# Optimization experiments

Hardware: AMD Instinct MI355X
Metric: run time of the kernel (lower is better)

## Reference

```python
import jax, jax.numpy as jnp
import numpy as np

N, E, F, H, RBF = 50000, 400000, 128, 8, 100
HD = F // H
CUTOFF = 6.0

def _xavier(k, shape):
    fan_out, fan_in = shape
    lim = (6.0 / (fan_in + fan_out)) ** 0.5
    return jax.random.uniform(k, shape, minval=-lim, maxval=lim, dtype=jnp.float32)

def setup_inputs():
    key = jax.random.key(0)
    ks = jax.random.split(key, 16)
    x = jax.random.normal(ks[0], (N, F), jnp.float32)
    vec = jax.random.normal(ks[1], (N, 3, F), jnp.float32)
    edge_index = jax.random.randint(ks[2], (2, E), 0, N, dtype=jnp.int32)
    r_ij = jax.random.uniform(ks[3], (E,), jnp.float32) * CUTOFF
    d_ij = jax.random.normal(ks[4], (E, 3), jnp.float32)
    d_ij = d_ij / jnp.linalg.norm(d_ij, axis=-1, keepdims=True)
    f_ij = jax.random.normal(ks[5], (E, RBF), jnp.float32)
    return dict(
        x=x, vec=vec, edge_index=edge_index, r_ij=r_ij, f_ij=f_ij, d_ij=d_ij,
        ln_w=jnp.ones((F,), jnp.float32), ln_b=jnp.zeros((F,), jnp.float32),
        Wq=_xavier(ks[6], (F, F)), bq=jnp.zeros((F,), jnp.float32),
        Wk=_xavier(ks[7], (F, F)), bk=jnp.zeros((F,), jnp.float32),
        Wv=_xavier(ks[8], (3 * F, F)), bv=jnp.zeros((3 * F,), jnp.float32),
        Wvec=_xavier(ks[9], (3 * F, F)), bvec=jnp.zeros((3 * F,), jnp.float32),
        Wo=_xavier(ks[10], (3 * F, F)), bo=jnp.zeros((3 * F,), jnp.float32),
        Wdk=_xavier(ks[11], (F, RBF)), bdk=jnp.zeros((F,), jnp.float32),
        Wdv=_xavier(ks[12], (3 * F, RBF)), bdv=jnp.zeros((3 * F,), jnp.float32),
    )

def _cutoff(r):
    # CosineCutoff with cutoff_lower=0
    return 0.5 * (jnp.cos(r * (jnp.pi / CUTOFF)) + 1.0) * (r < CUTOFF).astype(r.dtype)

def reference(x, vec, edge_index, r_ij, f_ij, d_ij, ln_w, ln_b, Wq, bq, Wk, bk,
              Wv, bv, Wvec, bvec, Wo, bo, Wdk, bdk, Wdv, bdv):
    src, dst = edge_index[0], edge_index[1]  # PyG: x_j = x[src], x_i = x[dst], aggregate at dst
    mu = x.mean(-1, keepdims=True)
    var = ((x - mu) ** 2).mean(-1, keepdims=True)
    xn = (x - mu) / jnp.sqrt(var + 1e-5) * ln_w + ln_b
    q = (xn @ Wq.T + bq).reshape(N, H, HD)
    k = (xn @ Wk.T + bk).reshape(N, H, HD)
    v = (xn @ Wv.T + bv).reshape(N, H, 3 * HD)
    vp = vec @ Wvec.T + bvec  # (N,3,3F)
    vec1, vec2, vec3 = vp[..., :F], vp[..., F:2 * F], vp[..., 2 * F:]
    vec_dot = (vec1 * vec2).sum(axis=1)  # (N,F)
    vec_h = vec.reshape(N, 3, H, HD)
    dk = jax.nn.silu(f_ij @ Wdk.T + bdk).reshape(E, H, HD)
    dv = jax.nn.silu(f_ij @ Wdv.T + bdv).reshape(E, H, 3 * HD)
    # edge-wise messages
    attn = jax.nn.silu((q[dst] * k[src] * dk).sum(-1)) * _cutoff(r_ij)[:, None]  # (E,H)
    v_j = v[src] * dv
    xm, v1m, v2m = v_j[..., :HD], v_j[..., HD:2 * HD], v_j[..., 2 * HD:]
    xm = xm * attn[..., None]  # (E,H,HD)
    vecm = vec_h[src] * v1m[:, None] + v2m[:, None] * d_ij[:, :, None, None]  # (E,3,H,HD)
    # scatter-add to destination nodes
    x_agg = jax.ops.segment_sum(xm.reshape(E, F), dst, num_segments=N)
    vec_agg = jax.ops.segment_sum(vecm.reshape(E, 3 * F), dst, num_segments=N).reshape(N, 3, F)
    o = x_agg @ Wo.T + bo
    o1, o2, o3 = o[:, :F], o[:, F:2 * F], o[:, 2 * F:]
    dx = vec_dot * o2 + o3
    dvec = vec3 * o1[:, None, :] + vec_agg
    return dx, dvec
```

## Files before the change

kernel.cpp:

```cpp
#include <hip/hip_runtime.h>

#define N_NODES 50000
#define N_EDGES 400000

typedef __bf16 bf16x8 __attribute__((ext_vector_type(8)));
typedef float f32x4 __attribute__((ext_vector_type(4)));

__device__ __forceinline__ float bflo(uint u){ union{uint i; float f;} v; v.i = u<<16; return v.f; }
__device__ __forceinline__ float bfhi(uint u){ union{uint i; float f;} v; v.i = u & 0xffff0000u; return v.f; }
__device__ __forceinline__ float bf2f(ushort u){ union{uint i; float f;} v; v.i = ((uint)u)<<16; return v.f; }
__device__ __forceinline__ ushort f2bf(float f){
  union{float f; uint i;} v; v.f = f;
  uint r = (v.i + 0x7fffu + ((v.i>>16)&1u))>>16;
  return (ushort)r;
}
__device__ __forceinline__ uint pack2(float a, float b){
  return (uint)f2bf(a) | ((uint)f2bf(b)<<16);
}

__global__ __launch_bounds__(256) void f32_to_bf16(
    const float* __restrict__ in, ushort* __restrict__ out, int n)
{
  int i = blockIdx.x*256 + threadIdx.x;
  if (i < n) out[i] = f2bf(in[i]);
}

__global__ __launch_bounds__(256) void ln_kernel(
    const float* __restrict__ x, const float* __restrict__ w,
    const float* __restrict__ b, ushort* __restrict__ xn)
{
  int n = blockIdx.x*4 + (threadIdx.x>>6);
  if (n >= N_NODES) return;
  int lane = threadIdx.x & 63;
  float2 xp = ((const float2*)x)[(size_t)n*64 + lane];
  float x0 = xp.x, x1 = xp.y;
  float s = x0 + x1, s2 = x0*x0 + x1*x1;
  #pragma unroll
  for (int off=1; off<64; off<<=1){ s += __shfl_xor(s,off); s2 += __shfl_xor(s2,off); }
  float mu  = s*(1.0f/128.0f);
  float var = s2*(1.0f/128.0f) - mu*mu;
  float inv = 1.0f/sqrtf(var + 1e-5f);
  float2 wp = ((const float2*)w)[lane];
  float2 bp = ((const float2*)b)[lane];
  float y0 = (x0-mu)*inv*wp.x + bp.x;
  float y1 = (x1-mu)*inv*wp.y + bp.y;
  ((uint*)xn)[(size_t)n*64 + lane] = pack2(y0, y1);
}

__global__ __launch_bounds__(256) void hist_kernel(
    const int* __restrict__ ei, int* __restrict__ cnt)
{
  int e = blockIdx.x*256 + threadIdx.x;
  if (e < N_EDGES) atomicAdd(&cnt[ei[N_EDGES + e]], 1);
}

__global__ __launch_bounds__(1024) void scan_kernel(
    const int* __restrict__ cnt, int* __restrict__ offs, int* __restrict__ cursor)
{
  __shared__ int wsum[16];
  __shared__ int carry_s;
  int tid = threadIdx.x, lane = tid & 63, wid = tid >> 6;
  if (tid == 0) carry_s = 0;
  __syncthreads();
  for (int base = 0; base < N_NODES; base += 1024){
    int i = base + tid;
    int v = (i < N_NODES) ? cnt[i] : 0;
    int x = v;
    #pragma unroll
    for (int o=1;o<64;o<<=1){ int t=__shfl_up(x,o); if (lane>=o) x+=t; }
    if (lane == 63) wsum[wid] = x;
    __syncthreads();
    if (wid == 0){
      int ws = (lane < 16) ? wsum[lane] : 0;
      #pragma unroll
      for (int o=1;o<16;o<<=1){ int t=__shfl_up(ws,o); if (lane>=o) ws+=t; }
      if (lane < 16) wsum[lane] = ws;
    }
    __syncthreads();
    int wpre = (wid > 0) ? wsum[wid-1] : 0;
    int exc = x + wpre - v;
    int total = wsum[15];
    int o_ = carry_s + exc;
    if (i < N_NODES){ offs[i] = o_; cursor[i] = o_; }
    __syncthreads();
    if (tid == 0) carry_s += total;
    __syncthreads();
  }
  if (tid == 0) offs[N_NODES] = carry_s;
}

__global__ __launch_bounds__(256) void scatter_kernel(
    const int* __restrict__ ei, int* __restrict__ cursor,
    int* __restrict__ perm, int* __restrict__ srcs)
{
  int e = blockIdx.x*256 + threadIdx.x;
  if (e >= N_EDGES) return;
  int d = ei[N_EDGES + e];
  int pos = atomicAdd(&cursor[d], 1);
  perm[pos] = e;
  srcs[pos] = ei[e];
}

#define LDP 40

template<int MODE, int AF32>
__global__ __launch_bounds__(256) void gemm_bt(
    const void* __restrict__ Av, const ushort* __restrict__ W,
    const ushort* __restrict__ W2,
    const float* __restrict__ bias, const float* __restrict__ bias2,
    void* Cptr, const void* aux1, void* aux2,
    int M, int K, int Nc, const int* __restrict__ ridx)
{
  __shared__ ushort As[128*LDP];
  __shared__ ushort Bs[128*LDP];
  __shared__ ushort Bs2[(MODE==7) ? 128*LDP : 2];
  const int tid = threadIdx.x;
  const int row0 = blockIdx.x*128, col0 = blockIdx.y*128;
  const int wave = tid>>6, lane = tid&63;
  const int wm = (wave>>1)*64, wn = (wave&1)*64;
  const int lr = lane&15, lq = lane>>4;
  f32x4 acc[4][4] = {};
  f32x4 acc2[4][4] = {};

  for (int k0=0; k0<K; k0+=32){
    #pragma unroll
    for (int rnd=0; rnd<2; rnd++){
      int e4 = (rnd*256 + tid)*8;
      int r = e4>>5, c = e4&31;
      int gk = k0 + c;
      {
        int gr = row0 + r;
        uint2 lo, hi;
        if (AF32){
          const float* Af = (const float*)Av;
          int ga = gr;
          if (ridx && gr < M) ga = ridx[gr];
          if (gr < M && gk + 8 <= K){
            const float* p = Af + (size_t)ga*K + gk;
            float4 f0 = *(const float4*)p;
            float4 f1 = *(const float4*)(p+4);
            lo = make_uint2(pack2(f0.x,f0.y), pack2(f0.z,f0.w));
            hi = make_uint2(pack2(f1.x,f1.y), pack2(f1.z,f1.w));
          } else {
            float t[8];
            #pragma unroll
            for (int i=0;i<8;i++) t[i] = (gr<M && gk+i<K) ? Af[(size_t)ga*K + gk + i] : 0.0f;
            lo = make_uint2(pack2(t[0],t[1]), pack2(t[2],t[3]));
            hi = make_uint2(pack2(t[4],t[5]), pack2(t[6],t[7]));
          }
        } else {
          const ushort* Ab = (const ushort*)Av;
          if (gr < M && gk + 8 <= K){
            const ushort* p = Ab + (size_t)gr*K + gk;
            lo = *(const uint2*)p; hi = *(const uint2*)(p+4);
          } else {
            ushort t[8];
            #pragma unroll
            for (int i=0;i<8;i++) t[i] = (gr<M && gk+i<K) ? Ab[(size_t)gr*K + gk + i] : (ushort)0;
            lo = make_uint2(((uint)t[0])|((uint)t[1]<<16), ((uint)t[2])|((uint)t[3]<<16));
            hi = make_uint2(((uint)t[4])|((uint)t[5]<<16), ((uint)t[6])|((uint)t[7]<<16));
          }
        }
        *(uint2*)&As[r*LDP + c]     = lo;
        *(uint2*)&As[r*LDP + c + 4] = hi;
      }
      {
        int gr = col0 + r;
        uint2 lo, hi;
        if (gr < Nc && gk + 8 <= K){
          const ushort* p = W + (size_t)gr*K + gk;
          lo = *(const uint2*)p; hi = *(const uint2*)(p+4);
        } else {
          ushort t[8];
          #pragma unroll
          for (int i=0;i<8;i++) t[i] = (gr<Nc && gk+i<K) ? W[(size_t)gr*K + gk + i] : (ushort)0;
          lo = make_uint2(((uint)t[0])|((uint)t[1]<<16), ((uint)t[2])|((uint)t[3]<<16));
          hi = make_uint2(((uint)t[4])|((uint)t[5]<<16), ((uint)t[6])|((uint)t[7]<<16));
        }
        *(uint2*)&Bs[r*LDP + c]     = lo;
        *(uint2*)&Bs[r*LDP + c + 4] = hi;
      }
      if (MODE==7){
        int gr = col0 + r;
        uint2 lo, hi;
        if (gr < Nc && gk + 8 <= K){
          const ushort* p = W2 + (size_t)gr*K + gk;
          lo = *(const uint2*)p; hi = *(const uint2*)(p+4);
        } else {
          ushort t[8];
          #pragma unroll
          for (int i=0;i<8;i++) t[i] = (gr<Nc && gk+i<K) ? W2[(size_t)gr*K + gk + i] : (ushort)0;
          lo = make_uint2(((uint)t[0])|((uint)t[1]<<16), ((uint)t[2])|((uint)t[3]<<16));
          hi = make_uint2(((uint)t[4])|((uint)t[5]<<16), ((uint)t[6])|((uint)t[7]<<16));
        }
        *(uint2*)&Bs2[r*LDP + c]     = lo;
        *(uint2*)&Bs2[r*LDP + c + 4] = hi;
      }
    }
    __syncthreads();
    bf16x8 af[4], bfr[4];
    #pragma unroll
    for (int i=0;i<4;i++) af[i]  = *(const bf16x8*)&As[(wm + i*16 + lr)*LDP + lq*8];
    #pragma unroll
    for (int i=0;i<4;i++) bfr[i] = *(const bf16x8*)&Bs[(wn + i*16 + lr)*LDP + lq*8];
    #pragma unroll
    for (int i=0;i<4;i++)
      #pragma unroll
      for (int j=0;j<4;j++)
        acc[i][j] = __builtin_amdgcn_mfma_f32_16x16x32_bf16(af[i], bfr[j], acc[i][j], 0,0,0);
    if (MODE==7){
      bf16x8 bfr2[4];
      #pragma unroll
      for (int i=0;i<4;i++) bfr2[i] = *(const bf16x8*)&Bs2[(wn + i*16 + lr)*LDP + lq*8];
      #pragma unroll
      for (int i=0;i<4;i++)
        #pragma unroll
        for (int j=0;j<4;j++)
          acc2[i][j] = __builtin_amdgcn_mfma_f32_16x16x32_bf16(af[i], bfr2[j], acc2[i][j], 0,0,0);
    }
    __syncthreads();
  }

  const ushort* aux1b = (const ushort*)aux1;
  const float*  aux1f = (const float*)aux1;
  float* aux2f = (float*)aux2;

  #pragma unroll
  for (int i=0;i<4;i++){
    int rowb = row0 + wm + i*16 + lq*4;
    #pragma unroll
    for (int j=0;j<4;j++){
      int c = col0 + wn + j*16 + lr;
      float bv  = bias  ? bias[c]  : 0.0f;
      float bv2 = (MODE==7) ? bias2[c] : 0.0f;
      #pragma unroll
      for (int rg=0; rg<4; rg++){
        int row = rowb + rg;
        if (row < M){
          float vv = acc[i][j][rg] + bv;
          size_t idx = (size_t)row*Nc + c;
          if (MODE==0){
            ((ushort*)Cptr)[idx] = f2bf(vv);
          } else if (MODE==1){
            vv = vv/(1.0f + __expf(-vv));
            ((ushort*)Cptr)[idx] = f2bf(vv);
          } else if (MODE==4){
            aux2f[idx] *= vv;
          } else if (MODE==5){
            float r = aux1f[idx] + vv;
            ((float*)Cptr)[idx] = r;
          } else if (MODE==6){
            float o1 = bf2f(aux1b[(size_t)(row/3)*Nc + c]);
            float r = vv*o1 + aux2f[idx];
            ((float*)Cptr)[idx] = r;
          } else if (MODE==7){
            float vv2 = acc2[i][j][rg] + bv2;
            atomicAdd(aux2f + (size_t)(row/3)*Nc + c, vv*vv2);
          }
        }
      }
    }
  }
}

__global__ __launch_bounds__(256) void agg_kernel(
    int st, int len,
    const int* __restrict__ offs, const int* __restrict__ srcs,
    const int* __restrict__ perm,
    const float* __restrict__ rij, const float* __restrict__ dij,
    const ushort* __restrict__ qk, const ushort* __restrict__ v,
    const ushort* __restrict__ vecb, const ushort* __restrict__ dkv,
    float* __restrict__ x_agg, float* __restrict__ vec_agg)
{
  int n = blockIdx.x*4 + (threadIdx.x>>6);
  if (n >= N_NODES) return;
  int lane = threadIdx.x & 63;
  int s0 = offs[n], s1 = offs[n+1];
  int hi = st + len;
  int a0 = s0 > st ? s0 : st;
  int a1 = s1 < hi ? s1 : hi;
  if (a0 >= a1) return;

  const uint* qk32  = (const uint*)qk;
  const uint* v32   = (const uint*)v;
  const uint* vec32 = (const uint*)vecb;
  const uint* dkv32 = (const uint*)dkv;
  uint qp = qk32[(size_t)n*128 + lane];
  int h  = lane>>3;
  int cb = h*24 + (lane&7);

  float xa0=0.f, xa1=0.f;
  float vA0=0.f, vA1=0.f, vB0=0.f, vB1=0.f, vC0=0.f, vC1=0.f;

  for (int p=a0; p<a1; ++p){
    int src = srcs[p];
    int eo  = perm[p];
    uint kp = qk32[(size_t)src*128 + 64 + lane];
    const uint* dr = dkv32 + (size_t)(p-st)*256;
    uint dkp = dr[lane];
    float s = bflo(qp)*bflo(kp)*bflo(dkp) + bfhi(qp)*bfhi(kp)*bfhi(dkp);
    s += __shfl_xor(s,1); s += __shfl_xor(s,2); s += __shfl_xor(s,4);
    float r = rij[eo];
    float cut = (r < 6.0f) ? 0.5f*(__cosf(r*0.52359877559829887f) + 1.0f) : 0.0f;
    float attn = (s/(1.0f + __expf(-s))) * cut;

    size_t vr = (size_t)src*192;
    const uint* dv = dr + 64;
    uint vx = v32[vr+cb],    dvx = dv[cb];
    uint v1 = v32[vr+cb+8],  dv1 = dv[cb+8];
    uint v2 = v32[vr+cb+16], dv2 = dv[cb+16];
    xa0 += bflo(vx)*bflo(dvx)*attn;
    xa1 += bfhi(vx)*bfhi(dvx)*attn;
    float v1m0 = bflo(v1)*bflo(dv1), v1m1 = bfhi(v1)*bfhi(dv1);
    float v2m0 = bflo(v2)*bflo(dv2), v2m1 = bfhi(v2)*bfhi(dv2);
    float d0 = dij[3*(size_t)eo], d1 = dij[3*(size_t)eo+1], d2 = dij[3*(size_t)eo+2];
    uint va  = vec32[vr + lane];
    uint vbx = vec32[vr + 64 + lane];
    uint vc  = vec32[vr + 128 + lane];
    vA0 += bflo(va)*v1m0  + v2m0*d0;  vA1 += bfhi(va)*v1m1  + v2m1*d0;
    vB0 += bflo(vbx)*v1m0 + v2m0*d1;  vB1 += bfhi(vbx)*v1m1 + v2m1*d1;
    vC0 += bflo(vc)*v1m0  + v2m0*d2;  vC1 += bfhi(vc)*v1m1  + v2m1*d2;
  }

  int f0 = 2*lane;
  float* xrow = x_agg + (size_t)n*128;
  atomicAdd(xrow+f0,   xa0);
  atomicAdd(xrow+f0+1, xa1);
  float* vrow = vec_agg + (size_t)n*384;
  atomicAdd(vrow+f0,       vA0); atomicAdd(vrow+f0+1,     vA1);
  atomicAdd(vrow+128+f0,   vB0); atomicAdd(vrow+128+f0+1, vB1);
  atomicAdd(vrow+256+f0,   vC0); atomicAdd(vrow+256+f0+1, vC1);
}

extern "C" void kernel_launch(void* const* d_in, const int* in_sizes, int n_in,
                              void* d_out, int out_size, void* d_ws, size_t ws_size,
                              hipStream_t stream)
{
  (void)in_sizes; (void)n_in; (void)out_size;
  constexpr int Nn = N_NODES, Ee = N_EDGES;
  const float* x    = (const float*)d_in[0];
  const float* vec  = (const float*)d_in[1];
  const int*   eidx = (const int*)  d_in[2];
  const float* rij  = (const float*)d_in[3];
  const float* fij  = (const float*)d_in[4];
  const float* dij  = (const float*)d_in[5];
  const float* lnw  = (const float*)d_in[6];
  const float* lnb  = (const float*)d_in[7];
  const float* Wq   = (const float*)d_in[8];
  const float* bq   = (const float*)d_in[9];
  const float* Wk   = (const float*)d_in[10];
  const float* bk   = (const float*)d_in[11];
  const float* Wv   = (const float*)d_in[12];
  const float* bv   = (const float*)d_in[13];
  const float* Wvec = (const float*)d_in[14];
  const float* bvec = (const float*)d_in[15];
  const float* Wo   = (const float*)d_in[16];
  const float* bo   = (const float*)d_in[17];
  const float* Wdk  = (const float*)d_in[18];
  const float* bdk  = (const float*)d_in[19];
  const float* Wdv  = (const float*)d_in[20];
  const float* bdv  = (const float*)d_in[21];

  float*  outf = (float*)d_out;
  ushort* qkb  = (ushort*)d_out;
  float*  vdot = outf;
  float*  vagg = outf + (size_t)Nn*128;

  char* w = (char*)d_ws;
  size_t off = 0;
  auto alloc = [&](size_t bytes){ size_t o = off; off += (bytes + 255) & ~(size_t)255; return o; };

  ushort* WqkB  = (ushort*)(w + alloc(32768*2));
  ushort* WvB   = (ushort*)(w + alloc(49152*2));
  ushort* WvecB = (ushort*)(w + alloc(49152*2));
  ushort* WoB   = (ushort*)(w + alloc(49152*2));
  ushort* WdkvB = (ushort*)(w + alloc(51200*2));
  float*  bqk   = (float*) (w + alloc(256*4));
  float*  bdkv  = (float*) (w + alloc(512*4));
  ushort* vecb  = (ushort*)(w + alloc((size_t)3*Nn*128*2));
  ushort* vb    = (ushort*)(w + alloc((size_t)Nn*384*2));
  float*  xagg  = (float*) (w + alloc((size_t)Nn*128*4));
  ushort* o1b   = (ushort*)(w + alloc((size_t)Nn*128*2));
  int*    cnt   = (int*)   (w + alloc((size_t)Nn*4));
  int*    offs  = (int*)   (w + alloc((size_t)(Nn+1)*4));
  int*    cursor= (int*)   (w + alloc((size_t)Nn*4));
  int*    perm  = (int*)   (w + alloc((size_t)Ee*4));
  int*    srcs  = (int*)   (w + alloc((size_t)Ee*4));

  size_t sc_off = off;
  char*  sc = w + sc_off;
  ushort* xn = (ushort*)sc;
  long long chunkC = (ws_size > sc_off) ? (long long)((ws_size - sc_off) / 1024) : 64;
  if (chunkC > Ee) chunkC = Ee;
  chunkC &= ~63LL;
  if (chunkC < 64) chunkC = 64;
  ushort* dkvc = (ushort*)sc;

  f32_to_bf16<<<(16384+255)/256, 256, 0, stream>>>(Wq,   WqkB,        16384);
  f32_to_bf16<<<(16384+255)/256, 256, 0, stream>>>(Wk,   WqkB+16384,  16384);
  f32_to_bf16<<<(49152+255)/256, 256, 0, stream>>>(Wv,   WvB,   49152);
  f32_to_bf16<<<(49152+255)/256, 256, 0, stream>>>(Wvec, WvecB, 49152);
  f32_to_bf16<<<(49152+255)/256, 256, 0, stream>>>(Wo,   WoB,   49152);
  f32_to_bf16<<<(12800+255)/256, 256, 0, stream>>>(Wdk,  WdkvB,       12800);
  f32_to_bf16<<<(38400+255)/256, 256, 0, stream>>>(Wdv,  WdkvB+12800, 38400);
  f32_to_bf16<<<(3*Nn*128+255)/256, 256, 0, stream>>>(vec, vecb, 3*Nn*128);
  hipMemcpyAsync(bqk,        bq,  128*4, hipMemcpyDeviceToDevice, stream);
  hipMemcpyAsync(bqk + 128,  bk,  128*4, hipMemcpyDeviceToDevice, stream);
  hipMemcpyAsync(bdkv,       bdk, 128*4, hipMemcpyDeviceToDevice, stream);
  hipMemcpyAsync(bdkv + 128, bdv, 384*4, hipMemcpyDeviceToDevice, stream);

  hipMemsetAsync(xagg, 0, (size_t)Nn*128*4, stream);
  hipMemsetAsync(vagg, 0, (size_t)3*Nn*128*4, stream);
  hipMemsetAsync(cnt,  0, (size_t)Nn*4, stream);

  hist_kernel<<<(Ee+255)/256, 256, 0, stream>>>(eidx, cnt);
  scan_kernel<<<1, 1024, 0, stream>>>(cnt, offs, cursor);
  scatter_kernel<<<(Ee+255)/256, 256, 0, stream>>>(eidx, cursor, perm, srcs);

  ln_kernel<<<(Nn+3)/4, 256, 0, stream>>>(x, lnw, lnb, xn);

  gemm_bt<0,0><<<dim3((Nn+127)/128, 2), 256, 0, stream>>>(xn, WqkB, nullptr, bqk, nullptr, qkb, nullptr, nullptr, Nn, 128, 256, nullptr);
  gemm_bt<0,0><<<dim3((Nn+127)/128, 3), 256, 0, stream>>>(xn, WvB,  nullptr, bv,  nullptr, vb,  nullptr, nullptr, Nn, 128, 384, nullptr);

  for (int st = 0; st < Ee; st += (int)chunkC){
    int len = Ee - st; if (len > (int)chunkC) len = (int)chunkC;
    gemm_bt<1,1><<<dim3((len+127)/128, 4), 256, 0, stream>>>(fij, WdkvB, nullptr, bdkv, nullptr, dkvc, nullptr, nullptr, len, 100, 512, perm + st);
    agg_kernel<<<(Nn+3)/4, 256, 0, stream>>>(st, len, offs, srcs, perm, rij, dij, qkb, vb, vecb, dkvc, xagg, vagg);
  }

  hipMemsetAsync(vdot, 0, (size_t)Nn*128*4, stream);
  gemm_bt<7,0><<<dim3((3*Nn+127)/128, 1), 256, 0, stream>>>(vecb, WvecB, WvecB + 128*128, bvec, bvec + 128, nullptr, nullptr, vdot, 3*Nn, 128, 128, nullptr);

  gemm_bt<0,1><<<dim3((Nn+127)/128, 1), 256, 0, stream>>>(xagg, WoB,            nullptr, bo,       nullptr, o1b,    nullptr, nullptr, Nn, 128, 128, nullptr);
  gemm_bt<4,1><<<dim3((Nn+127)/128, 1), 256, 0, stream>>>(xagg, WoB + 128*128,  nullptr, bo + 128, nullptr, nullptr, nullptr, vdot,   Nn, 128, 128, nullptr);
  gemm_bt<5,1><<<dim3((Nn+127)/128, 1), 256, 0, stream>>>(xagg, WoB + 256*128,  nullptr, bo + 256, nullptr, outf,   vdot,    nullptr, Nn, 128, 128, nullptr);
  gemm_bt<6,0><<<dim3((3*Nn+127)/128, 1), 256, 0, stream>>>(vecb, WvecB + 256*128, nullptr, bvec + 256, nullptr, outf + (size_t)Nn*128, o1b, vagg, 3*Nn, 128, 128, nullptr);
}
```

Before: 1.637 ms.

## Gather f_ij to padded bf16, balance edge aggregation by fixed edge groups

Adds a gather kernel that writes permuted f_ij rows to a K=128 zero-padded bf16 buffer, so the dk/dv GEMM reads contiguous bf16 with padded weights and no indirect f32 row loads. The GEMM gains an XCD-aware block swizzle and uses 16-byte global/LDS copies. The scatter kernel now stores dst and a packed (r, d) float4 per sorted edge. The aggregation kernel switches from one wave per node to one wave per 16 consecutive sorted edges, flushing atomics whenever the destination changes. This evens out load across high- and low-degree nodes, at the cost of more atomics and an extra pass over f_ij.

```diff
diff --git a/kernel.cpp b/kernel.cpp
--- a/kernel.cpp
+++ b/kernel.cpp
@@ -23,6 +23,16 @@
 {
   int i = blockIdx.x*256 + threadIdx.x;
   if (i < n) out[i] = f2bf(in[i]);
+}
+
+__global__ __launch_bounds__(256) void convert_pad(
+    const float* __restrict__ in, ushort* __restrict__ out,
+    int rows, int Kin, int Kout)
+{
+  int i = blockIdx.x*256 + threadIdx.x;
+  if (i >= rows*Kout) return;
+  int r = i / Kout, c = i - r*Kout;
+  out[i] = (c < Kin) ? f2bf(in[(size_t)r*Kin + c]) : (ushort)0;
 }
 
 __global__ __launch_bounds__(256) void ln_kernel(
@@ -90,8 +100,10 @@
 }
 
 __global__ __launch_bounds__(256) void scatter_kernel(
-    const int* __restrict__ ei, int* __restrict__ cursor,
-    int* __restrict__ perm, int* __restrict__ srcs)
+    const int* __restrict__ ei, const float* __restrict__ rij,
+    const float* __restrict__ dij, int* __restrict__ cursor,
+    int* __restrict__ perm, int* __restrict__ srcs, int* __restrict__ dsts,
+    float4* __restrict__ ed)
 {
   int e = blockIdx.x*256 + threadIdx.x;
   if (e >= N_EDGES) return;
@@ -99,23 +111,52 @@
   int pos = atomicAdd(&cursor[d], 1);
   perm[pos] = e;
   srcs[pos] = ei[e];
+  dsts[pos] = d;
+  ed[pos] = make_float4(rij[e], dij[3*(size_t)e], dij[3*(size_t)e+1], dij[3*(size_t)e+2]);
+}
+
+__global__ __launch_bounds__(256) void gather_fij(
+    int st, int len, const int* __restrict__ perm,
+    const float* __restrict__ fij, ushort* __restrict__ out)
+{
+  int p = blockIdx.x*4 + (threadIdx.x>>6);
+  if (p >= len) return;
+  int lane = threadIdx.x & 63;
+  int eo = perm[st + p];
+  uint val = 0;
+  if (lane < 50){
+    float2 f = *(const float2*)(fij + (size_t)eo*100 + 2*lane);
+    val = pack2(f.x, f.y);
+  }
+  ((uint*)out)[(size_t)p*64 + lane] = val;
 }
 
 #define LDP 40
 
-template<int MODE, int AF32>
+template<int MODE, int AF32, int SWZ>
 __global__ __launch_bounds__(256) void gemm_bt(
     const void* __restrict__ Av, const ushort* __restrict__ W,
     const ushort* __restrict__ W2,
     const float* __restrict__ bias, const float* __restrict__ bias2,
     void* Cptr, const void* aux1, void* aux2,
-    int M, int K, int Nc, const int* __restrict__ ridx)
+    int M, int K, int Nc)
 {
   __shared__ ushort As[128*LDP];
   __shared__ ushort Bs[128*LDP];
   __shared__ ushort Bs2[(MODE==7) ? 128*LDP : 2];
   const int tid = threadIdx.x;
-  const int row0 = blockIdx.x*128, col0 = blockIdx.y*128;
+  int bx, by;
+  if (SWZ){
+    int nby = Nc >> 7;
+    int nwg = gridDim.x;
+    int id  = blockIdx.x;
+    int q = nwg >> 3, r = nwg & 7;
+    int xcd = id & 7, iq = id >> 3;
+    int base = (xcd < r) ? xcd*(q+1) : r*(q+1) + (xcd - r)*q;
+    int L = base + iq;
+    bx = L / nby; by = L - bx*nby;
+  } else { bx = blockIdx.x; by = blockIdx.y; }
+  const int row0 = bx*128, col0 = by*128;
   const int wave = tid>>6, lane = tid&63;
   const int wm = (wave>>1)*64, wn = (wave&1)*64;
   const int lr = lane&15, lq = lane>>4;
@@ -130,13 +171,11 @@
       int gk = k0 + c;
       {
         int gr = row0 + r;
-        uint2 lo, hi;
         if (AF32){
           const float* Af = (const float*)Av;
-          int ga = gr;
-          if (ridx && gr < M) ga = ridx[gr];
+          uint2 lo, hi;
           if (gr < M && gk + 8 <= K){
-            const float* p = Af + (size_t)ga*K + gk;
+            const float* p = Af + (size_t)gr*K + gk;
             float4 f0 = *(const float4*)p;
             float4 f1 = *(const float4*)(p+4);
             lo = make_uint2(pack2(f0.x,f0.y), pack2(f0.z,f0.w));
@@ -144,57 +183,51 @@
           } else {
             float t[8];
             #pragma unroll
-            for (int i=0;i<8;i++) t[i] = (gr<M && gk+i<K) ? Af[(size_t)ga*K + gk + i] : 0.0f;
+            for (int i=0;i<8;i++) t[i] = (gr<M && gk+i<K) ? Af[(size_t)gr*K + gk + i] : 0.0f;
             lo = make_uint2(pack2(t[0],t[1]), pack2(t[2],t[3]));
             hi = make_uint2(pack2(t[4],t[5]), pack2(t[6],t[7]));
           }
+          *(uint2*)&As[r*LDP + c]     = lo;
+          *(uint2*)&As[r*LDP + c + 4] = hi;
         } else {
           const ushort* Ab = (const ushort*)Av;
           if (gr < M && gk + 8 <= K){
-            const ushort* p = Ab + (size_t)gr*K + gk;
-            lo = *(const uint2*)p; hi = *(const uint2*)(p+4);
+            uint4 t = *(const uint4*)(Ab + (size_t)gr*K + gk);
+            *(uint4*)&As[r*LDP + c] = t;
           } else {
             ushort t[8];
             #pragma unroll
             for (int i=0;i<8;i++) t[i] = (gr<M && gk+i<K) ? Ab[(size_t)gr*K + gk + i] : (ushort)0;
-            lo = make_uint2(((uint)t[0])|((uint)t[1]<<16), ((uint)t[2])|((uint)t[3]<<16));
-            hi = make_uint2(((uint)t[4])|((uint)t[5]<<16), ((uint)t[6])|((uint)t[7]<<16));
+            *(uint2*)&As[r*LDP + c]     = make_uint2(((uint)t[0])|((uint)t[1]<<16), ((uint)t[2])|((uint)t[3]<<16));
+            *(uint2*)&As[r*LDP + c + 4] = make_uint2(((uint)t[4])|((uint)t[5]<<16), ((uint)t[6])|((uint)t[7]<<16));
           }
         }
-        *(uint2*)&As[r*LDP + c]     = lo;
-        *(uint2*)&As[r*LDP + c + 4] = hi;
       }
       {
         int gr = col0 + r;
-        uint2 lo, hi;
         if (gr < Nc && gk + 8 <= K){
-          const ushort* p = W + (size_t)gr*K + gk;
-          lo = *(const uint2*)p; hi = *(const uint2*)(p+4);
+          uint4 t = *(const uint4*)(W + (size_t)gr*K + gk);
+          *(uint4*)&Bs[r*LDP + c] = t;
         } else {
           ushort t[8];
           #pragma unroll
           for (int i=0;i<8;i++) t[i] = (gr<Nc && gk+i<K) ? W[(size_t)gr*K + gk + i] : (ushort)0;
-          lo = make_uint2(((uint)t[0])|((uint)t[1]<<16), ((uint)t[2])|((uint)t[3]<<16));
-          hi = make_uint2(((uint)t[4])|((uint)t[5]<<16), ((uint)t[6])|((uint)t[7]<<16));
+          *(uint2*)&Bs[r*LDP + c]     = make_uint2(((uint)t[0])|((uint)t[1]<<16), ((uint)t[2])|((uint)t[3]<<16));
+          *(uint2*)&Bs[r*LDP + c + 4] = make_uint2(((uint)t[4])|((uint)t[5]<<16), ((uint)t[6])|((uint)t[7]<<16));
         }
-        *(uint2*)&Bs[r*LDP + c]     = lo;
-        *(uint2*)&Bs[r*LDP + c + 4] = hi;
       }
       if (MODE==7){
         int gr = col0 + r;
-        uint2 lo, hi;
         if (gr < Nc && gk + 8 <= K){
-          const ushort* p = W2 + (size_t)gr*K + gk;
-          lo = *(const uint2*)p; hi = *(const uint2*)(p+4);
+          uint4 t = *(const uint4*)(W2 + (size_t)gr*K + gk);
+          *(uint4*)&Bs2[r*LDP + c] = t;
         } else {
           ushort t[8];
           #pragma unroll
           for (int i=0;i<8;i++) t[i] = (gr<Nc && gk+i<K) ? W2[(size_t)gr*K + gk + i] : (ushort)0;
-          lo = make_uint2(((uint)t[0])|((uint)t[1]<<16), ((uint)t[2])|((uint)t[3]<<16));
-          hi = make_uint2(((uint)t[4])|((uint)t[5]<<16), ((uint)t[6])|((uint)t[7]<<16));
+          *(uint2*)&Bs2[r*LDP + c]     = make_uint2(((uint)t[0])|((uint)t[1]<<16), ((uint)t[2])|((uint)t[3]<<16));
+          *(uint2*)&Bs2[r*LDP + c + 4] = make_uint2(((uint)t[4])|((uint)t[5]<<16), ((uint)t[6])|((uint)t[7]<<16));
         }
-        *(uint2*)&Bs2[r*LDP + c]     = lo;
-        *(uint2*)&Bs2[r*LDP + c + 4] = hi;
       }
     }
     __syncthreads();
@@ -263,44 +296,60 @@
   }
 }
 
+#define AGG_G 16
+
 __global__ __launch_bounds__(256) void agg_kernel(
     int st, int len,
-    const int* __restrict__ offs, const int* __restrict__ srcs,
-    const int* __restrict__ perm,
-    const float* __restrict__ rij, const float* __restrict__ dij,
+    const int* __restrict__ dsts, const int* __restrict__ srcs,
+    const float4* __restrict__ ed,
     const ushort* __restrict__ qk, const ushort* __restrict__ v,
     const ushort* __restrict__ vecb, const ushort* __restrict__ dkv,
     float* __restrict__ x_agg, float* __restrict__ vec_agg)
 {
-  int n = blockIdx.x*4 + (threadIdx.x>>6);
-  if (n >= N_NODES) return;
+  int w = blockIdx.x*4 + (threadIdx.x>>6);
+  int p0 = st + w*AGG_G;
+  int pend = st + len;
+  if (p0 >= pend) return;
+  int p1 = p0 + AGG_G; if (p1 > pend) p1 = pend;
   int lane = threadIdx.x & 63;
-  int s0 = offs[n], s1 = offs[n+1];
-  int hi = st + len;
-  int a0 = s0 > st ? s0 : st;
-  int a1 = s1 < hi ? s1 : hi;
-  if (a0 >= a1) return;
 
   const uint* qk32  = (const uint*)qk;
   const uint* v32   = (const uint*)v;
   const uint* vec32 = (const uint*)vecb;
   const uint* dkv32 = (const uint*)dkv;
-  uint qp = qk32[(size_t)n*128 + lane];
   int h  = lane>>3;
   int cb = h*24 + (lane&7);
-
+  int f0 = 2*lane;
+
+  int dcur = -1;
+  uint qp = 0;
   float xa0=0.f, xa1=0.f;
   float vA0=0.f, vA1=0.f, vB0=0.f, vB1=0.f, vC0=0.f, vC1=0.f;
 
-  for (int p=a0; p<a1; ++p){
+  for (int p=p0; p<p1; ++p){
+    int d = dsts[p];
+    if (d != dcur){
+      if (dcur >= 0){
+        float* xrow = x_agg + (size_t)dcur*128;
+        atomicAdd(xrow+f0,   xa0);
+        atomicAdd(xrow+f0+1, xa1);
+        float* vrow = vec_agg + (size_t)dcur*384;
+        atomicAdd(vrow+f0,       vA0); atomicAdd(vrow+f0+1,     vA1);
+        atomicAdd(vrow+128+f0,   vB0); atomicAdd(vrow+128+f0+1, vB1);
+        atomicAdd(vrow+256+f0,   vC0); atomicAdd(vrow+256+f0+1, vC1);
+      }
+      dcur = d;
+      qp = qk32[(size_t)d*128 + lane];
+      xa0=xa1=vA0=vA1=vB0=vB1=vC0=vC1=0.f;
+    }
     int src = srcs[p];
-    int eo  = perm[p];
+    float4 e = ed[p];
     uint kp = qk32[(size_t)src*128 + 64 + lane];
     const uint* dr = dkv32 + (size_t)(p-st)*256;
     uint dkp = dr[lane];
     float s = bflo(qp)*bflo(kp)*bflo(dkp) + bfhi(qp)*bfhi(kp)*bfhi(dkp);
     s += __shfl_xor(s,1); s += __shfl_xor(s,2); s += __shfl_xor(s,4);
-    float r = rij[eo];
+    float r = e.x;
     float cut = (r < 6.0f) ? 0.5f*(__cosf(r*0.52359877559829887f) + 1.0f) : 0.0f;
     float attn = (s/(1.0f + __expf(-s))) * cut;
 
@@ -313,23 +362,22 @@
     xa1 += bfhi(vx)*bfhi(dvx)*attn;
     float v1m0 = bflo(v1)*bflo(dv1), v1m1 = bfhi(v1)*bfhi(dv1);
     float v2m0 = bflo(v2)*bflo(dv2), v2m1 = bfhi(v2)*bfhi(dv2);
-    float d0 = dij[3*(size_t)eo], d1 = dij[3*(size_t)eo+1], d2 = dij[3*(size_t)eo+2];
     uint va  = vec32[vr + lane];
     uint vbx = vec32[vr + 64 + lane];
     uint vc  = vec32[vr + 128 + lane];
-    vA0 += bflo(va)*v1m0  + v2m0*d0;  vA1 += bfhi(va)*v1m1  + v2m1*d0;
-    vB0 += bflo(vbx)*v1m0 + v2m0*d1;  vB1 += bfhi(vbx)*v1m1 + v2m1*d1;
-    vC0 += bflo(vc)*v1m0  + v2m0*d2;  vC1 += bfhi(vc)*v1m1  + v2m1*d2;
-  }
-
-  int f0 = 2*lane;
-  float* xrow = x_agg + (size_t)n*128;
-  atomicAdd(xrow+f0,   xa0);
-  atomicAdd(xrow+f0+1, xa1);
-  float* vrow = vec_agg + (size_t)n*384;
-  atomicAdd(vrow+f0,       vA0); atomicAdd(vrow+f0+1,     vA1);
-  atomicAdd(vrow+128+f0,   vB0); atomicAdd(vrow+128+f0+1, vB1);
-  atomicAdd(vrow+256+f0,   vC0); atomicAdd(vrow+256+f0+1, vC1);
+    vA0 += bflo(va)*v1m0  + v2m0*e.y;  vA1 += bfhi(va)*v1m1  + v2m1*e.y;
+    vB0 += bflo(vbx)*v1m0 + v2m0*e.z;  vB1 += bfhi(vbx)*v1m1 + v2m1*e.z;
+    vC0 += bflo(vc)*v1m0  + v2m0*e.w;  vC1 += bfhi(vc)*v1m1  + v2m1*e.w;
+  }
+  if (dcur >= 0){
+    float* xrow = x_agg + (size_t)dcur*128;
+    atomicAdd(xrow+f0,   xa0);
+    atomicAdd(xrow+f0+1, xa1);
+    float* vrow = vec_agg + (size_t)dcur*384;
+    atomicAdd(vrow+f0,       vA0); atomicAdd(vrow+f0+1,     vA1);
+    atomicAdd(vrow+128+f0,   vB0); atomicAdd(vrow+128+f0+1, vB1);
+    atomicAdd(vrow+256+f0,   vC0); atomicAdd(vrow+256+f0+1, vC1);
+  }
 }
 
 extern "C" void kernel_launch(void* const* d_in, const int* in_sizes, int n_in,
@@ -374,7 +422,7 @@
   ushort* WvB   = (ushort*)(w + alloc(49152*2));
   ushort* WvecB = (ushort*)(w + alloc(49152*2));
   ushort* WoB   = (ushort*)(w + alloc(49152*2));
-  ushort* WdkvB = (ushort*)(w + alloc(51200*2));
+  ushort* WdkvP = (ushort*)(w + alloc(512*128*2));
   float*  bqk   = (float*) (w + alloc(256*4));
   float*  bdkv  = (float*) (w + alloc(512*4));
   ushort* vecb  = (ushort*)(w + alloc((size_t)3*Nn*128*2));
@@ -386,23 +434,26 @@
   int*    cursor= (int*)   (w + alloc((size_t)Nn*4));
   int*    perm  = (int*)   (w + alloc((size_t)Ee*4));
   int*    srcs  = (int*)   (w + alloc((size_t)Ee*4));
+  int*    dsts  = (int*)   (w + alloc((size_t)Ee*4));
+  float4* ed    = (float4*)(w + alloc((size_t)Ee*16));
 
   size_t sc_off = off;
   char*  sc = w + sc_off;
   ushort* xn = (ushort*)sc;
-  long long chunkC = (ws_size > sc_off) ? (long long)((ws_size - sc_off) / 1024) : 64;
-  if (chunkC > Ee) chunkC = Ee;
-  chunkC &= ~63LL;
-  if (chunkC < 64) chunkC = 64;
-  ushort* dkvc = (ushort*)sc;
+  long long chunkC = (ws_size > sc_off) ? (long long)((ws_size - sc_off) / 1280) : 128;
+  if (chunkC > 98304) chunkC = 98304;
+  chunkC &= ~127LL;
+  if (chunkC < 128) chunkC = 128;
+  ushort* fijb = (ushort*)sc;
+  ushort* dkvc = (ushort*)(sc + (size_t)chunkC*256);
 
   f32_to_bf16<<<(16384+255)/256, 256, 0, stream>>>(Wq,   WqkB,        16384);
   f32_to_bf16<<<(16384+255)/256, 256, 0, stream>>>(Wk,   WqkB+16384,  16384);
   f32_to_bf16<<<(49152+255)/256, 256, 0, stream>>>(Wv,   WvB,   49152);
   f32_to_bf16<<<(49152+255)/256, 256, 0, stream>>>(Wvec, WvecB, 49152);
   f32_to_bf16<<<(49152+255)/256, 256, 0, stream>>>(Wo,   WoB,   49152);
-  f32_to_bf16<<<(12800+255)/256, 256, 0, stream>>>(Wdk,  WdkvB,       12800);
-  f32_to_bf16<<<(38400+255)/256, 256, 0, stream>>>(Wdv,  WdkvB+12800, 38400);
+  convert_pad<<<(128*128+255)/256, 256, 0, stream>>>(Wdk, WdkvP,           128, 100, 128);
+  convert_pad<<<(384*128+255)/256, 256, 0, stream>>>(Wdv, WdkvP + 128*128, 384, 100, 128);
   f32_to_bf16<<<(3*Nn*128+255)/256, 256, 0, stream>>>(vec, vecb, 3*Nn*128);
   hipMemcpyAsync(bqk,        bq,  128*4, hipMemcpyDeviceToDevice, stream);
   hipMemcpyAsync(bqk + 128,  bk,  128*4, hipMemcpyDeviceToDevice, stream);
@@ -415,24 +466,27 @@
 
   hist_kernel<<<(Ee+255)/256, 256, 0, stream>>>(eidx, cnt);
   scan_kernel<<<1, 1024, 0, stream>>>(cnt, offs, cursor);
-  scatter_kernel<<<(Ee+255)/256, 256, 0, stream>>>(eidx, cursor, perm, srcs);
+  scatter_kernel<<<(Ee+255)/256, 256, 0, stream>>>(eidx, rij, dij, cursor, perm, srcs, dsts, ed);
 
   ln_kernel<<<(Nn+3)/4, 256, 0, stream>>>(x, lnw, lnb, xn);
 
-  gemm_bt<0,0><<<dim3((Nn+127)/128, 2), 256, 0, stream>>>(xn, WqkB, nullptr, bqk, nullptr, qkb, nullptr, nullptr, Nn, 128, 256, nullptr);
-  gemm_bt<0,0><<<dim3((Nn+127)/128, 3), 256, 0, stream>>>(xn, WvB,  nullptr, bv,  nullptr, vb,  nullptr, nullptr, Nn, 128, 384, nullptr);
+  gemm_bt<0,0,0><<<dim3((Nn+127)/128, 2), 256, 0, stream>>>(xn, WqkB, nullptr, bqk, nullptr, qkb, nullptr, nullptr, Nn, 128, 256);
+  gemm_bt<0,0,0><<<dim3((Nn+127)/128, 3), 256, 0, stream>>>(xn, WvB,  nullptr, bv,  nullptr, vb,  nullptr, nullptr, Nn, 128, 384);
 
   for (int st = 0; st < Ee; st += (int)chunkC){
     int len = Ee - st; if (len > (int)chunkC) len = (int)chunkC;
-    gemm_bt<1,1><<<dim3((len+127)/128, 4), 256, 0, stream>>>(fij, WdkvB, nullptr, bdkv, nullptr, dkvc, nullptr, nullptr, len, 100, 512, perm + st);
-    agg_kernel<<<(Nn+3)/4, 256, 0, stream>>>(st, len, offs, srcs, perm, rij, dij, qkb, vb, vecb, dkvc, xagg, vagg);
+    gather_fij<<<(len+3)/4, 256, 0, stream>>>(st, len, perm, fij, fijb);
+    int nbx = (len+127)/128;
+    gemm_bt<1,0,1><<<dim3(nbx*4, 1), 256, 0, stream>>>(fijb, WdkvP, nullptr, bdkv, nullptr, dkvc, nullptr, nullptr, len, 128, 512);
+    int waves = (len + AGG_G - 1)/AGG_G;
+    agg_kernel<<<(waves+3)/4, 256, 0, stream>>>(st, len, dsts, srcs, ed, qkb, vb, vecb, dkvc, xagg, vagg);
   }
 
   hipMemsetAsync(vdot, 0, (size_t)Nn*128*4, stream);
-  gemm_bt<7,0><<<dim3((3*Nn+127)/128, 1), 256, 0, stream>>>(vecb, WvecB, WvecB + 128*128, bvec, bvec + 128, nullptr, nullptr, vdot, 3*Nn, 128, 128, nullptr);
-
-  gemm_bt<0,1><<<dim3((Nn+127)/128, 1), 256, 0, stream>>>(xagg, WoB,            nullptr, bo,       nullptr, o1b,    nullptr, nullptr, Nn, 128, 128, nullptr);
-  gemm_bt<4,1><<<dim3((Nn+127)/128, 1), 256, 0, stream>>>(xagg, WoB + 128*128,  nullptr, bo + 128, nullptr, nullptr, nullptr, vdot,   Nn, 128, 128, nullptr);
-  gemm_bt<5,1><<<dim3((Nn+127)/128, 1), 256, 0, stream>>>(xagg, WoB + 256*128,  nullptr, bo + 256, nullptr, outf,   vdot,    nullptr, Nn, 128, 128, nullptr);
-  gemm_bt<6,0><<<dim3((3*Nn+127)/128, 1), 256, 0, stream>>>(vecb, WvecB + 256*128, nullptr, bvec + 256, nullptr, outf + (size_t)Nn*128, o1b, vagg, 3*Nn, 128, 128, nullptr);
-}
+  gemm_bt<7,0,0><<<dim3((3*Nn+127)/128, 1), 256, 0, stream>>>(vecb, WvecB, WvecB + 128*128, bvec, bvec + 128, nullptr, nullptr, vdot, 3*Nn, 128, 128);
+
+  gemm_bt<0,1,0><<<dim3((Nn+127)/128, 1), 256, 0, stream>>>(xagg, WoB,            nullptr, bo,       nullptr, o1b,    nullptr, nullptr, Nn, 128, 128);
+  gemm_bt<4,1,0><<<dim3((Nn+127)/128, 1), 256, 0, stream>>>(xagg, WoB + 128*128,  nullptr, bo + 128, nullptr, nullptr, nullptr, vdot,   Nn, 128, 128);
+  gemm_bt<5,1,0><<<dim3((Nn+127)/128, 1), 256, 0, stream>>>(xagg, WoB + 256*128,  nullptr, bo + 256, nullptr, outf,   vdot,    nullptr, Nn, 128, 128);
+  gemm_bt<6,0,0><<<dim3((3*Nn+127)/128, 1), 256, 0, stream>>>(vecb, WvecB + 256*128, nullptr, bvec + 256, nullptr, outf + (size_t)Nn*128, o1b, vagg, 3*Nn, 128, 128);
+}
```

Result: no change. 1.616 ms (-1.3%).
